# Kernel optimization log

Hardware: AMD Instinct MI355X
Metric: run time of the kernel (lower is better)

## Reference

```python
import jax, jax.numpy as jnp
import numpy as np

T, D, O, E, R = 16384, 4096, 4096, 8, 64  # tokens, in_feat, out_feat, n_adapters, max_rank


def setup_inputs() -> dict:
    key = jax.random.key(0)
    ks = jax.random.split(key, 6)
    x = jax.random.normal(ks[0], (T, D), jnp.float32)
    base_output = jax.random.normal(ks[1], (T, O), jnp.float32)
    A = jax.random.normal(ks[2], (E, D, R), jnp.float32) * 0.02  # loraA per adapter
    B = jax.random.normal(ks[3], (E, R, O), jnp.float32) * 0.02  # loraB per adapter
    scaling = jax.random.uniform(ks[4], (E,), jnp.float32, 0.5, 2.0)  # lora_alpha/rank per adapter
    adapter_ids = jax.random.randint(ks[5], (T,), 0, E, dtype=jnp.int32)  # per-token routing
    return {"x": x, "base_output": base_output, "A": A, "B": B,
            "scaling": scaling, "adapter_ids": adapter_ids}


def reference(x, base_output, A, B, scaling, adapter_ids):
    """S-LoRA batched multi-adapter forward: out = base + (x @ A_i) @ B_i * s_i,
    with adapter i routed per token. Expressed as E masked low-rank GEMMs
    (loop over the small fixed adapter set, vectorized over tokens)."""
    out = base_output
    for e in range(E):
        gate = (adapter_ids == e).astype(x.dtype) * scaling[e]  # (T,)
        h = x @ A[e]                                            # (T, R)
        out = out + (h @ B[e]) * gate[:, None]                  # (T, O)
    return out
```

## Files before the change

kernel.cpp:

```cpp
#include <hip/hip_runtime.h>

#define TT 16384
#define DD 4096
#define OO 4096
#define NE 8
#define RRK 64

typedef _Float16 f16x8 __attribute__((ext_vector_type(8)));
typedef float f32x4 __attribute__((ext_vector_type(4)));

#define CNT_OFF 0
#define PERM_OFF 1024
#define AT_OFF (1u << 20)
#define BT_OFF (5u << 20)
#define H_OFF (9u << 20)

typedef const __attribute__((address_space(1))) void GPTR;
typedef __attribute__((address_space(3))) void LPTR;
#define GLOAD16(g, l) __builtin_amdgcn_global_load_lds((GPTR*)(g), (LPTR*)(l), 16, 0, 0)

__global__ void prep_kernel(const int* __restrict__ ids,
                            const float* __restrict__ A,
                            const float* __restrict__ B,
                            int* __restrict__ cnt,
                            int* __restrict__ perm,
                            _Float16* __restrict__ At,
                            _Float16* __restrict__ Bt) {
  const int bid = blockIdx.x, tid = threadIdx.x;
  if (bid < 64) {
    int t = bid * 256 + tid;
    int e = ids[t];
    int pos = atomicAdd(&cnt[e], 1);
    perm[e * TT + pos] = t;
    return;
  }
  __shared__ float tile[64][65];
  if (bid < 576) {
    int idx = bid - 64;
    int e = idx >> 6, kb = (idx & 63) << 6;
    #pragma unroll
    for (int i = 0; i < 16; ++i) {
      int lin = i * 256 + tid;
      int kr = lin >> 6, r = lin & 63;
      tile[kr][r] = A[((size_t)e * DD + kb + kr) * RRK + r];
    }
    __syncthreads();
    #pragma unroll
    for (int i = 0; i < 16; ++i) {
      int lin = i * 256 + tid;
      int r = lin >> 6, kk = lin & 63;
      At[((size_t)e * RRK + r) * DD + kb + kk] = (_Float16)tile[kk][r];
    }
  } else {
    int idx = bid - 576;
    int e = idx >> 6, ob = (idx & 63) << 6;
    #pragma unroll
    for (int i = 0; i < 16; ++i) {
      int lin = i * 256 + tid;
      int r = lin >> 6, o = lin & 63;
      tile[r][o] = B[((size_t)e * RRK + r) * OO + ob + o];
    }
    __syncthreads();
    #pragma unroll
    for (int i = 0; i < 16; ++i) {
      int lin = i * 256 + tid;
      int o = lin >> 6, r2 = lin & 63;
      Bt[((size_t)e * OO + ob + o) * RRK + r2] = (_Float16)tile[r2][o];
    }
  }
}

#define S1_GRID 320
__global__ __launch_bounds__(256, 2)
void lora_stage1(const float* __restrict__ x,
                 const _Float16* __restrict__ At,
                 const float* __restrict__ scaling,
                 const int* __restrict__ cnt,
                 const int* __restrict__ perm,
                 _Float16* __restrict__ H) {
  __shared__ float Xs[2][4096];
  __shared__ _Float16 As[2][4096];
  __shared__ int toks[64];
  __shared__ int tokc[64];
  const int tid = threadIdx.x;
  const int lane = tid & 63, w = tid >> 6;
  const int lr = lane & 15, g = lane >> 4;
  const int s = lr & 7;
  const int mr = w * 16 + lr;

  const int sgx = (tid & 15) ^ ((tid >> 4) & 7);
  const int sga = (tid & 7) ^ ((tid >> 3) & 7);

  int tiles = 0;
  #pragma unroll
  for (int ee = 0; ee < NE; ++ee) tiles += (cnt[ee] + 63) >> 6;

  for (int wi = blockIdx.x; wi < tiles; wi += S1_GRID) {
    int e = 0, base = 0, n_e = 0;
    {
      int acc0 = 0;
      #pragma unroll
      for (int ee = 0; ee < NE; ++ee) {
        int c = cnt[ee];
        int tl = (c + 63) >> 6;
        if (wi >= acc0 && wi < acc0 + tl) { e = ee; base = acc0; n_e = c; }
        acc0 += tl;
      }
    }
    int m0 = (wi - base) << 6;

    if (tid < 64) {
      int rloc = m0 + tid;
      int v = (rloc < n_e) ? perm[e * TT + rloc] : -1;
      toks[tid] = v;
      tokc[tid] = (v < 0) ? perm[e * TT + n_e - 1] : v;
    }
    __syncthreads();

    const float* xsrc[4];
    #pragma unroll
    for (int p = 0; p < 4; ++p)
      xsrc[p] = x + (size_t)tokc[p * 16 + (tid >> 4)] * DD + sgx * 4;
    const _Float16* asrc = At + ((size_t)e * RRK + (tid >> 3)) * DD + sga * 8;
    int otok[4];
    #pragma unroll
    for (int rg = 0; rg < 4; ++rg) otok[rg] = toks[w * 16 + g * 4 + rg];

    f32x4 acc[4] = {};

    #pragma unroll
    for (int p = 0; p < 4; ++p)
      GLOAD16(xsrc[p], (char*)Xs[0] + p * 4096 + tid * 16);
    #pragma unroll
    for (int p = 0; p < 2; ++p)
      GLOAD16(asrc + (size_t)p * 32 * DD, (char*)As[0] + p * 4096 + tid * 16);
    __syncthreads();

    for (int it = 0; it < 64; ++it) {
      int cur = it & 1;
      int kb = (it + 1) << 6;
      if (it < 63) {
        #pragma unroll
        for (int p = 0; p < 4; ++p)
          GLOAD16(xsrc[p] + kb, (char*)Xs[cur ^ 1] + p * 4096 + tid * 16);
        #pragma unroll
        for (int p = 0; p < 2; ++p)
          GLOAD16(asrc + (size_t)p * 32 * DD + kb, (char*)As[cur ^ 1] + p * 4096 + tid * 16);
      }

      const f32x4* xr = (const f32x4*)Xs[cur];
      const f16x8* ar = (const f16x8*)As[cur];
      #pragma unroll
      for (int ks = 0; ks < 2; ++ks) {
        f32x4 a0 = xr[mr * 16 + ((2 * g + 8 * ks) ^ s)];
        f32x4 a1 = xr[mr * 16 + ((2 * g + 8 * ks + 1) ^ s)];
        f16x8 xa;
        #pragma unroll
        for (int i = 0; i < 4; ++i) {
          xa[i] = (_Float16)a0[i];
          xa[4 + i] = (_Float16)a1[i];
        }
        #pragma unroll
        for (int nf = 0; nf < 4; ++nf) {
          f16x8 bfr = ar[(nf * 16 + lr) * 8 + ((g + 4 * ks) ^ s)];
          acc[nf] = __builtin_amdgcn_mfma_f32_16x16x32_f16(xa, bfr, acc[nf], 0, 0, 0);
        }
      }
      __syncthreads();
    }

    float sc = scaling[e];
    #pragma unroll
    for (int rg = 0; rg < 4; ++rg) {
      int tk = otok[rg];
      if (tk >= 0) {
        #pragma unroll
        for (int nf = 0; nf < 4; ++nf) {
          H[(size_t)tk * RRK + nf * 16 + lr] = (_Float16)(acc[nf][rg] * sc);
        }
      }
    }
  }
}

#define S2_GRID 4096
__global__ __launch_bounds__(256, 4)
void lora_stage2(const float* __restrict__ baseo,
                 const _Float16* __restrict__ Bt,
                 const _Float16* __restrict__ H,
                 const int* __restrict__ cnt,
                 const int* __restrict__ perm,
                 float* __restrict__ out) {
  const int tid = threadIdx.x;
  const int lane = tid & 63, w = tid >> 6;
  const int lr = lane & 15;
  const int g = lane >> 4;
  const int kq = g << 3;
  const int g4 = g << 2;

  int tot = 0;
  #pragma unroll
  for (int ee = 0; ee < NE; ++ee) tot += ((cnt[ee] + 63) >> 6) << 4;

  for (int wi = blockIdx.x; wi < tot; wi += S2_GRID) {
    int e = 0, base = 0, n_e = 0;
    {
      int acc0 = 0;
      #pragma unroll
      for (int ee = 0; ee < NE; ++ee) {
        int c = cnt[ee];
        int work = ((c + 63) >> 6) << 4;
        if (wi >= acc0 && wi < acc0 + work) { e = ee; base = acc0; n_e = c; }
        acc0 += work;
      }
    }
    int local = wi - base;
    int tiles_m = (n_e + 63) >> 6;
    int mt = local % tiles_m;
    int nt = local / tiles_m;
    int m0 = mt << 6, o0 = nt << 8;

    int row = m0 + w * 16 + lr;
    bool valid = row < n_e;
    int tk = perm[e * TT + (valid ? row : n_e - 1)];

    const _Float16* hp = H + (size_t)tk * RRK + kq;
    f16x8 hf0 = *(const f16x8*)(hp);
    f16x8 hf1 = *(const f16x8*)(hp + 32);

    const _Float16* bp = Bt + ((size_t)e * OO + o0 + lr) * RRK + kq;

    f32x4 acc[16];
    #pragma unroll
    for (int of = 0; of < 16; ++of) acc[of] = (f32x4){0.f, 0.f, 0.f, 0.f};

    #pragma unroll
    for (int of = 0; of < 16; ++of) {
      f16x8 b0 = *(const f16x8*)(bp + (size_t)of * 16 * RRK);
      f16x8 b1 = *(const f16x8*)(bp + (size_t)of * 16 * RRK + 32);
      acc[of] = __builtin_amdgcn_mfma_f32_16x16x32_f16(b0, hf0, acc[of], 0, 0, 0);
      acc[of] = __builtin_amdgcn_mfma_f32_16x16x32_f16(b1, hf1, acc[of], 0, 0, 0);
    }

    if (valid) {
      size_t rowoff = (size_t)tk * OO + o0 + g4;
      #pragma unroll
      for (int h = 0; h < 2; ++h) {
        float4 bv[8];
        #pragma unroll
        for (int j = 0; j < 8; ++j)
          bv[j] = *(const float4*)(baseo + rowoff + (size_t)(h * 8 + j) * 16);
        #pragma unroll
        for (int j = 0; j < 8; ++j) {
          int of = h * 8 + j;
          float4 r4;
          r4.x = bv[j].x + acc[of][0];
          r4.y = bv[j].y + acc[of][1];
          r4.z = bv[j].z + acc[of][2];
          r4.w = bv[j].w + acc[of][3];
          *(float4*)(out + rowoff + (size_t)of * 16) = r4;
        }
      }
    }
  }
}

extern "C" void kernel_launch(void* const* d_in, const int* in_sizes, int n_in,
                              void* d_out, int out_size, void* d_ws, size_t ws_size,
                              hipStream_t stream) {
  const float* x = (const float*)d_in[0];
  const float* baseo = (const float*)d_in[1];
  const float* A = (const float*)d_in[2];
  const float* B = (const float*)d_in[3];
  const float* scaling = (const float*)d_in[4];
  const int* ids = (const int*)d_in[5];
  float* out = (float*)d_out;
  char* ws = (char*)d_ws;

  int* cnt = (int*)(ws + CNT_OFF);
  int* perm = (int*)(ws + PERM_OFF);
  _Float16* At = (_Float16*)(ws + AT_OFF);
  _Float16* Bt = (_Float16*)(ws + BT_OFF);
  _Float16* H = (_Float16*)(ws + H_OFF);

  hipMemsetAsync(cnt, 0, NE * sizeof(int), stream);
  hipLaunchKernelGGL(prep_kernel, dim3(1088), dim3(256), 0, stream,
                     ids, A, B, cnt, perm, At, Bt);
  hipLaunchKernelGGL(lora_stage1, dim3(S1_GRID), dim3(256), 0, stream,
                     x, At, scaling, cnt, perm, H);
  hipLaunchKernelGGL(lora_stage2, dim3(S2_GRID), dim3(256), 0, stream,
                     baseo, Bt, H, cnt, perm, out);
}
```

Baseline: 325.0 us.

## Shrink stage-1 token tiles to 16 rows, stage x via registers as fp16, aggregate histogram atomics

Stage 1 now processes 16-token tiles instead of 64. Each wave computes one 16-column slice of the rank dimension. The x rows are loaded into registers and converted to fp16 before being written to swizzled LDS, replacing fp32 direct-to-LDS loads. LDS use drops, so the launch bound rises to 4 blocks per SM and the grid grows to 1024 to raise occupancy. In exchange, each At tile is reloaded four times as often across blocks. The prep kernel also builds a per-block histogram in shared memory, so each block issues one global atomic per adapter instead of one per token.

Measured after the change: 304.3 us. 6.4% less time.

```diff
diff --git a/kernel.cpp b/kernel.cpp
--- a/kernel.cpp
+++ b/kernel.cpp
@@ -7,6 +7,7 @@
 #define RRK 64
 
 typedef _Float16 f16x8 __attribute__((ext_vector_type(8)));
+typedef _Float16 f16x4 __attribute__((ext_vector_type(4)));
 typedef float f32x4 __attribute__((ext_vector_type(4)));
 
 #define CNT_OFF 0
@@ -28,9 +29,16 @@
                             _Float16* __restrict__ Bt) {
   const int bid = blockIdx.x, tid = threadIdx.x;
   if (bid < 64) {
+    __shared__ int h1[NE], h2[NE], bases[NE];
+    if (tid < NE) { h1[tid] = 0; h2[tid] = 0; }
+    __syncthreads();
     int t = bid * 256 + tid;
     int e = ids[t];
-    int pos = atomicAdd(&cnt[e], 1);
+    atomicAdd(&h1[e], 1);
+    __syncthreads();
+    if (tid < NE) bases[tid] = atomicAdd(&cnt[tid], h1[tid]);
+    __syncthreads();
+    int pos = bases[e] + atomicAdd(&h2[e], 1);
     perm[e * TT + pos] = t;
     return;
   }
@@ -70,30 +78,30 @@
   }
 }
 
-#define S1_GRID 320
-__global__ __launch_bounds__(256, 2)
+#define S1_GRID 1024
+__global__ __launch_bounds__(256, 4)
 void lora_stage1(const float* __restrict__ x,
                  const _Float16* __restrict__ At,
                  const float* __restrict__ scaling,
                  const int* __restrict__ cnt,
                  const int* __restrict__ perm,
                  _Float16* __restrict__ H) {
-  __shared__ float Xs[2][4096];
   __shared__ _Float16 As[2][4096];
-  __shared__ int toks[64];
-  __shared__ int tokc[64];
+  __shared__ _Float16 Xs[2][1024];
+  __shared__ int toks[16];
   const int tid = threadIdx.x;
   const int lane = tid & 63, w = tid >> 6;
   const int lr = lane & 15, g = lane >> 4;
-  const int s = lr & 7;
-  const int mr = w * 16 + lr;
-
-  const int sgx = (tid & 15) ^ ((tid >> 4) & 7);
-  const int sga = (tid & 7) ^ ((tid >> 3) & 7);
+
+  const int arow = tid >> 3;
+  const int agr = (tid & 7) ^ ((tid >> 3) & 7);
+  const int xrow = tid >> 4;
+  const int xbyte = xrow * 128 + ((((tid & 15) >> 1) ^ (xrow & 7)) << 4) + ((tid & 1) << 3);
+  const int fr_sw = lr & 7;
 
   int tiles = 0;
   #pragma unroll
-  for (int ee = 0; ee < NE; ++ee) tiles += (cnt[ee] + 63) >> 6;
+  for (int ee = 0; ee < NE; ++ee) tiles += (cnt[ee] + 15) >> 4;
 
   for (int wi = blockIdx.x; wi < tiles; wi += S1_GRID) {
     int e = 0, base = 0, n_e = 0;
@@ -102,69 +110,60 @@
       #pragma unroll
       for (int ee = 0; ee < NE; ++ee) {
         int c = cnt[ee];
-        int tl = (c + 63) >> 6;
+        int tl = (c + 15) >> 4;
         if (wi >= acc0 && wi < acc0 + tl) { e = ee; base = acc0; n_e = c; }
         acc0 += tl;
       }
     }
-    int m0 = (wi - base) << 6;
-
-    if (tid < 64) {
+    int m0 = (wi - base) << 4;
+
+    if (tid < 16) {
       int rloc = m0 + tid;
-      int v = (rloc < n_e) ? perm[e * TT + rloc] : -1;
-      toks[tid] = v;
-      tokc[tid] = (v < 0) ? perm[e * TT + n_e - 1] : v;
-    }
-    __syncthreads();
-
-    const float* xsrc[4];
-    #pragma unroll
-    for (int p = 0; p < 4; ++p)
-      xsrc[p] = x + (size_t)tokc[p * 16 + (tid >> 4)] * DD + sgx * 4;
-    const _Float16* asrc = At + ((size_t)e * RRK + (tid >> 3)) * DD + sga * 8;
-    int otok[4];
-    #pragma unroll
-    for (int rg = 0; rg < 4; ++rg) otok[rg] = toks[w * 16 + g * 4 + rg];
-
-    f32x4 acc[4] = {};
-
-    #pragma unroll
-    for (int p = 0; p < 4; ++p)
-      GLOAD16(xsrc[p], (char*)Xs[0] + p * 4096 + tid * 16);
-    #pragma unroll
-    for (int p = 0; p < 2; ++p)
-      GLOAD16(asrc + (size_t)p * 32 * DD, (char*)As[0] + p * 4096 + tid * 16);
+      toks[tid] = (rloc < n_e) ? perm[e * TT + rloc] : -1;
+    }
+    __syncthreads();
+
+    int stok = toks[xrow];
+    if (stok < 0) stok = toks[0];
+    const float* xsrc = x + (size_t)stok * DD + ((tid & 15) << 2);
+    const _Float16* asrc = At + ((size_t)e * RRK + arow) * DD + agr * 8;
+
+    f32x4 acc = {};
+
+    {
+      float4 v = *(const float4*)(xsrc);
+      GLOAD16(asrc, (char*)As[0] + tid * 16);
+      GLOAD16(asrc + (size_t)32 * DD, (char*)As[0] + 4096 + tid * 16);
+      f16x4 cv;
+      cv[0] = (_Float16)v.x; cv[1] = (_Float16)v.y;
+      cv[2] = (_Float16)v.z; cv[3] = (_Float16)v.w;
+      *(f16x4*)((char*)Xs[0] + xbyte) = cv;
+    }
     __syncthreads();
 
     for (int it = 0; it < 64; ++it) {
       int cur = it & 1;
-      int kb = (it + 1) << 6;
+      float4 vn;
       if (it < 63) {
-        #pragma unroll
-        for (int p = 0; p < 4; ++p)
-          GLOAD16(xsrc[p] + kb, (char*)Xs[cur ^ 1] + p * 4096 + tid * 16);
-        #pragma unroll
-        for (int p = 0; p < 2; ++p)
-          GLOAD16(asrc + (size_t)p * 32 * DD + kb, (char*)As[cur ^ 1] + p * 4096 + tid * 16);
-      }
-
-      const f32x4* xr = (const f32x4*)Xs[cur];
-      const f16x8* ar = (const f16x8*)As[cur];
+        int kb = (it + 1) << 6;
+        vn = *(const float4*)(xsrc + kb);
+        GLOAD16(asrc + kb, (char*)As[cur ^ 1] + tid * 16);
+        GLOAD16(asrc + (size_t)32 * DD + kb, (char*)As[cur ^ 1] + 4096 + tid * 16);
+      }
+
       #pragma unroll
       for (int ks = 0; ks < 2; ++ks) {
-        f32x4 a0 = xr[mr * 16 + ((2 * g + 8 * ks) ^ s)];
-        f32x4 a1 = xr[mr * 16 + ((2 * g + 8 * ks + 1) ^ s)];
-        f16x8 xa;
-        #pragma unroll
-        for (int i = 0; i < 4; ++i) {
-          xa[i] = (_Float16)a0[i];
-          xa[4 + i] = (_Float16)a1[i];
-        }
-        #pragma unroll
-        for (int nf = 0; nf < 4; ++nf) {
-          f16x8 bfr = ar[(nf * 16 + lr) * 8 + ((g + 4 * ks) ^ s)];
-          acc[nf] = __builtin_amdgcn_mfma_f32_16x16x32_f16(xa, bfr, acc[nf], 0, 0, 0);
-        }
+        int gr = (4 * ks + g) ^ fr_sw;
+        f16x8 xa = *(const f16x8*)((char*)Xs[cur] + lr * 128 + gr * 16);
+        f16x8 bf = *(const f16x8*)((char*)As[cur] + (w * 16 + lr) * 128 + gr * 16);
+        acc = __builtin_amdgcn_mfma_f32_16x16x32_f16(xa, bf, acc, 0, 0, 0);
+      }
+
+      if (it < 63) {
+        f16x4 cv;
+        cv[0] = (_Float16)vn.x; cv[1] = (_Float16)vn.y;
+        cv[2] = (_Float16)vn.z; cv[3] = (_Float16)vn.w;
+        *(f16x4*)((char*)Xs[cur ^ 1] + xbyte) = cv;
       }
       __syncthreads();
     }
@@ -172,14 +171,11 @@
     float sc = scaling[e];
     #pragma unroll
     for (int rg = 0; rg < 4; ++rg) {
-      int tk = otok[rg];
-      if (tk >= 0) {
-        #pragma unroll
-        for (int nf = 0; nf < 4; ++nf) {
-          H[(size_t)tk * RRK + nf * 16 + lr] = (_Float16)(acc[nf][rg] * sc);
-        }
-      }
-    }
+      int tk = toks[g * 4 + rg];
+      if (tk >= 0)
+        H[(size_t)tk * RRK + w * 16 + lr] = (_Float16)(acc[rg] * sc);
+    }
+    __syncthreads();
   }
 }
 
```
